# Kernel optimization log

Measured on AMD Instinct MI355X. Metric: run time of the kernel, lower is better.

## Reference

```python
import jax, jax.numpy as jnp
import numpy as np

N_NODES = 50000
N_EDGES = 800000
NFEATS = 256
HFEATS = 256
N_TARGET = 8
NEG_SLOPE = 0.2


def setup_inputs() -> dict:
    key = jax.random.key(0)
    ks = jax.random.split(key, 16)
    s = 1.0 / np.sqrt(HFEATS)
    inp = {
        'hv': jax.random.normal(ks[0], (N_NODES, NFEATS), dtype=jnp.float32),
        'src': jax.random.randint(ks[1], (N_EDGES,), 0, N_NODES, dtype=jnp.int32),
        'dst': jax.random.randint(ks[2], (N_EDGES,), 0, N_NODES, dtype=jnp.int32),
        'W_in': jax.random.normal(ks[3], (NFEATS, HFEATS), dtype=jnp.float32) * (1.0 / np.sqrt(NFEATS)),
        'b_in': jnp.zeros((HFEATS,), dtype=jnp.float32),
        'W_ro': jax.random.normal(ks[4], (3 * HFEATS, N_TARGET), dtype=jnp.float32) * (1.0 / np.sqrt(3 * HFEATS)),
        'b_ro': jnp.zeros((N_TARGET,), dtype=jnp.float32),
    }
    for i in range(1, 4):
        k = jax.random.split(ks[4 + i], 4)
        inp[f'fc{i}'] = jax.random.normal(k[0], (HFEATS, HFEATS), dtype=jnp.float32) * s
        inp[f'al{i}'] = jax.random.normal(k[1], (HFEATS,), dtype=jnp.float32) * s
        inp[f'ar{i}'] = jax.random.normal(k[2], (HFEATS,), dtype=jnp.float32) * s
        inp[f'bias{i}'] = jnp.zeros((HFEATS,), dtype=jnp.float32)
    return inp


def _gat(h, src, dst, fc, al, ar, bias):
    # DGL GATConv, 1 head: fc proj, additive attention, edge softmax over dst, sum agg.
    feat = h @ fc                                  # [N, H]
    el = feat @ al                                 # [N]
    er = feat @ ar                                 # [N]
    e = jax.nn.leaky_relu(el[src] + er[dst], NEG_SLOPE)   # [E]
    m = jax.ops.segment_max(e, dst, num_segments=N_NODES)
    ex = jnp.exp(e - m[dst])
    denom = jax.ops.segment_sum(ex, dst, num_segments=N_NODES)
    a = ex / denom[dst]                            # [E]
    out = jax.ops.segment_sum(feat[src] * a[:, None], dst, num_segments=N_NODES)
    return out + bias


def reference(hv, src, dst, W_in, b_in, W_ro, b_ro,
              fc1, al1, ar1, bias1, fc2, al2, ar2, bias2, fc3, al3, ar3, bias3):
    h0 = hv @ W_in + b_in
    h1 = _gat(jax.nn.relu(h0), src, dst, fc1, al1, ar1, bias1)
    h2 = _gat(jax.nn.relu(h1), src, dst, fc2, al2, ar2, bias2)
    h3 = _gat(jax.nn.relu(h2), src, dst, fc3, al3, ar3, bias3)
    out = jnp.concatenate([h1, h2, h3], axis=-1) @ W_ro + b_ro
    return jax.nn.sigmoid(out)
```

## Files before the change

kernel.cpp:

```cpp
#include <hip/hip_runtime.h>
#include <hip/hip_bf16.h>
#include <math.h>

#define NNODES 50000
#define NEDGES 800000
#define HF 256
#define NEG_SLOPE 0.2f
#define APAD 12288
#define CHUNK 3125
#define NBUCK 196
#define NG (NBUCK * 256)

typedef short bf16x8 __attribute__((ext_vector_type(8)));
typedef float f32x4 __attribute__((ext_vector_type(4)));
typedef float f32x2 __attribute__((ext_vector_type(2)));

__device__ __forceinline__ unsigned short f2bf(float f) {
  unsigned u = __float_as_uint(f);
  unsigned r = u + 0x7FFFu + ((u >> 16) & 1u);
  return (unsigned short)(r >> 16);
}
__device__ __forceinline__ float bf2f(unsigned short u) {
  return __uint_as_float((unsigned)u << 16);
}
__device__ __forceinline__ uint2 pack4(const float* v) {
  uint2 r;
  r.x = (unsigned)f2bf(v[0]) | ((unsigned)f2bf(v[1]) << 16);
  r.y = (unsigned)f2bf(v[2]) | ((unsigned)f2bf(v[3]) << 16);
  return r;
}
__device__ __forceinline__ uint4 pack8(const float* v) {
  uint4 r;
  r.x = (unsigned)f2bf(v[0]) | ((unsigned)f2bf(v[1]) << 16);
  r.y = (unsigned)f2bf(v[2]) | ((unsigned)f2bf(v[3]) << 16);
  r.z = (unsigned)f2bf(v[4]) | ((unsigned)f2bf(v[5]) << 16);
  r.w = (unsigned)f2bf(v[6]) | ((unsigned)f2bf(v[7]) << 16);
  return r;
}

__device__ __forceinline__ int permc(int p) {
  return (p & 192) | ((p & 3) << 4) | ((p & 63) >> 2);
}

#define GLOAD_LDS16(gsrc, ldst)                                                \
  __builtin_amdgcn_global_load_lds(                                           \
      (const __attribute__((address_space(1))) unsigned int*)(const void*)(gsrc), \
      (__attribute__((address_space(3))) unsigned int*)(void*)(ldst), 16, 0, 0)

__device__ __forceinline__ void slot_decode(int s, int& row, int& kb) {
  row = ((s >> 3) << 1) | (((s >> 2) & 1) ^ ((s >> 4) & 1));
  kb  = ((s & 1) ^ (row & 1)) | ((((s >> 1) & 1) ^ ((s >> 3) & 1)) << 1);
}

__global__ __launch_bounds__(256)
void conv_hv(const float* __restrict__ x, unsigned short* __restrict__ o) {
  size_t i = (size_t)(blockIdx.x * 256 + threadIdx.x) * 8;
  float4 a = *(const float4*)(x + i);
  float4 b = *(const float4*)(x + i + 4);
  float v[8] = {a.x, a.y, a.z, a.w, b.x, b.y, b.z, b.w};
  *(uint4*)(o + i) = pack8(v);
}

__global__ __launch_bounds__(256)
void conv_wt(const float* __restrict__ W0, const float* __restrict__ W1,
             const float* __restrict__ W2, const float* __restrict__ W3,
             unsigned short* __restrict__ WT) {
  int mat = blockIdx.y;
  const float* W = mat == 0 ? W0 : (mat == 1 ? W1 : (mat == 2 ? W2 : W3));
  int i = blockIdx.x * 256 + threadIdx.x;
  int n = i >> 8, p = i & 255;
  int k = (mat == 0) ? p : permc(p);
  WT[(size_t)mat * 65536 + i] = f2bf(W[(size_t)k * 256 + n]);
}

__global__ __launch_bounds__(256)
void conv_wro(const float* __restrict__ Wro, unsigned short* __restrict__ WroT) {
  int i = blockIdx.x * 256 + threadIdx.x;
  if (i >= 16 * 768) return;
  int n = i / 768, kk = i % 768;
  int part = kk >> 8, q = kk & 255;
  float v = (n < 8) ? Wro[(size_t)((part << 8) + permc(q)) * 8 + n] : 0.f;
  WroT[i] = f2bf(v);
}

template<bool BIAS_RELU, bool DOTS>
__global__ __launch_bounds__(256)
void gemm_bf16(const unsigned short* __restrict__ A, const unsigned short* __restrict__ WT,
               const float* __restrict__ bias,
               const float* __restrict__ al, const float* __restrict__ ar,
               void* __restrict__ Cv,
               float* __restrict__ el, float* __restrict__ er, int M) {
  __shared__ unsigned short As[2][64 * 32];
  __shared__ unsigned short Bs[2][256 * 32];
  __shared__ float sEl[64][4], sEr[64][4];
  const int t = threadIdx.x;
  const int lane = t & 63;
  const int w = t >> 6;
  const int wc = w * 64;
  const int brow = blockIdx.x * 64;

  f32x4 acc[4][4];
#pragma unroll
  for (int i = 0; i < 4; i++)
#pragma unroll
    for (int j = 0; j < 4; j++) acc[i][j] = (f32x4)(0.f);

  int rA, kA;
  slot_decode(w * 64 + lane, rA, kA);
  const unsigned short* aP = A + (size_t)(brow + rA) * 256 + kA * 8;
  const unsigned short* bP[4];
#pragma unroll
  for (int i = 0; i < 4; i++) {
    int rB, kB;
    slot_decode(w * 256 + i * 64 + lane, rB, kB);
    bP[i] = WT + (size_t)rB * 256 + kB * 8;
  }
  unsigned short* lA[2] = {&As[0][w * 512], &As[1][w * 512]};
  unsigned short* lB[2] = {&Bs[0][w * 2048], &Bs[1][w * 2048]};

#define STAGE(buf, kt)                                                         \
  do {                                                                         \
    GLOAD_LDS16(aP + (kt) * 32, lA[buf]);                                      \
    GLOAD_LDS16(bP[0] + (kt) * 32, lB[buf]);                                   \
    GLOAD_LDS16(bP[1] + (kt) * 32, lB[buf] + 512);                             \
    GLOAD_LDS16(bP[2] + (kt) * 32, lB[buf] + 1024);                            \
    GLOAD_LDS16(bP[3] + (kt) * 32, lB[buf] + 1536);                            \
  } while (0)

  const int fr = lane & 15, fq = lane >> 4;
  int ard[4], brd[4];
#pragma unroll
  for (int i = 0; i < 4; i++) {
    int rowA = i * 16 + fr;
    ard[i] = ((rowA * 64 + fq * 16) ^ ((rowA & 7) << 4));
    int rowB = wc + i * 16 + fr;
    brd[i] = ((rowB * 64 + fq * 16) ^ ((rowB & 7) << 4));
  }

  STAGE(0, 0);
  __syncthreads();
  int cur = 0;
#pragma unroll
  for (int kt = 0; kt < 8; kt++) {
    if (kt < 7) STAGE(cur ^ 1, kt + 1);
    bf16x8 af[4], bfr[4];
#pragma unroll
    for (int i = 0; i < 4; i++) {
      af[i]  = *(const bf16x8*)((const char*)As[cur] + ard[i]);
      bfr[i] = *(const bf16x8*)((const char*)Bs[cur] + brd[i]);
    }
#pragma unroll
    for (int i = 0; i < 4; i++)
#pragma unroll
      for (int j = 0; j < 4; j++)
        acc[i][j] = __builtin_amdgcn_mfma_f32_16x16x32_bf16(af[i], bfr[j], acc[i][j], 0, 0, 0);
    if (kt < 7) {
      __syncthreads();
      cur ^= 1;
    }
  }
#undef STAGE

#pragma unroll
  for (int i = 0; i < 4; i++) {
#pragma unroll
    for (int r = 0; r < 4; r++) {
      int row = brow + i * 16 + fq * 4 + r;
      if (row < M) {
        float v[4];
#pragma unroll
        for (int j = 0; j < 4; j++) {
          float x = acc[i][j][r];
          if (BIAS_RELU) x = fmaxf(x + bias[wc + j * 16 + fr], 0.f);
          v[j] = x;
        }
        if constexpr (DOTS) {
          int pk = __builtin_amdgcn_cvt_pk_fp8_f32(v[0], v[1], 0, false);
          pk = __builtin_amdgcn_cvt_pk_fp8_f32(v[2], v[3], pk, true);
          *(unsigned*)((unsigned char*)Cv + (size_t)row * 256 + wc + fr * 4) = (unsigned)pk;
        } else {
          *(uint2*)((unsigned short*)Cv + (size_t)row * 256 + wc + fr * 4) = pack4(v);
        }
      }
    }
  }

  if constexpr (DOTS) {
    float alv[4], arv[4];
#pragma unroll
    for (int j = 0; j < 4; j++) {
      int colj = wc + j * 16 + fr;
      alv[j] = al[colj];
      arv[j] = ar[colj];
    }
    float pel[16], per_[16];
#pragma unroll
    for (int i = 0; i < 4; i++)
#pragma unroll
      for (int r = 0; r < 4; r++) {
        float se = 0.f, sr = 0.f;
#pragma unroll
        for (int j = 0; j < 4; j++) {
          se = fmaf(acc[i][j][r], alv[j], se);
          sr = fmaf(acc[i][j][r], arv[j], sr);
        }
        pel[i * 4 + r] = se;
        per_[i * 4 + r] = sr;
      }
#pragma unroll
    for (int off = 1; off < 16; off <<= 1)
#pragma unroll
      for (int k = 0; k < 16; k++) {
        pel[k] += __shfl_xor(pel[k], off);
        per_[k] += __shfl_xor(per_[k], off);
      }
    if (fr == 0) {
#pragma unroll
      for (int i = 0; i < 4; i++)
#pragma unroll
        for (int r = 0; r < 4; r++) {
          int rl = i * 16 + fq * 4 + r;
          sEl[rl][w] = pel[i * 4 + r];
          sEr[rl][w] = per_[i * 4 + r];
        }
    }
    __syncthreads();
    if (t < 64) {
      int row = brow + t;
      if (row < M) {
        el[row] = sEl[t][0] + sEl[t][1] + sEl[t][2] + sEl[t][3];
        er[row] = sEr[t][0] + sEr[t][1] + sEr[t][2] + sEr[t][3];
      }
    }
  }
}

__global__ __launch_bounds__(256)
void hist_coarse(const int* __restrict__ dst, int* __restrict__ gh) {
  __shared__ int lh[NBUCK];
  const int t = threadIdx.x, blk = blockIdx.x;
  if (t < NBUCK) lh[t] = 0;
  __syncthreads();
  const int base = blk * CHUNK;
  for (int i = t; i < CHUNK; i += 256)
    atomicAdd(&lh[dst[base + i] >> 8], 1);
  __syncthreads();
  if (t < NBUCK) gh[t * 256 + blk] = lh[t];
}

__global__ __launch_bounds__(256)
void bsum2(const int* __restrict__ g, int* __restrict__ bsum) {
  __shared__ int sm[256];
  int t = threadIdx.x;
  sm[t] = g[blockIdx.x * 256 + t];
  __syncthreads();
  for (int off = 128; off; off >>= 1) {
    if (t < off) sm[t] += sm[t + off];
    __syncthreads();
  }
  if (t == 0) bsum[blockIdx.x] = sm[0];
}

__global__ __launch_bounds__(256)
void sscan2(const int* __restrict__ bsum, int* __restrict__ boff) {
  __shared__ int sm[256];
  int t = threadIdx.x;
  sm[t] = (t < NBUCK) ? bsum[t] : 0;
  __syncthreads();
  for (int o = 1; o < 256; o <<= 1) {
    int v = (t >= o) ? sm[t - o] : 0;
    __syncthreads();
    sm[t] += v;
    __syncthreads();
  }
  if (t < NBUCK) boff[t] = (t == 0) ? 0 : sm[t - 1];
}

__global__ __launch_bounds__(256)
void abase2(const int* __restrict__ g, const int* __restrict__ boff,
            int* __restrict__ abase) {
  __shared__ int sm[256];
  int t = threadIdx.x;
  int i = blockIdx.x * 256 + t;
  int v = g[i];
  sm[t] = v;
  __syncthreads();
  for (int o = 1; o < 256; o <<= 1) {
    int x = (t >= o) ? sm[t - o] : 0;
    __syncthreads();
    sm[t] += x;
    __syncthreads();
  }
  abase[i] = boff[blockIdx.x] + sm[t] - v;
}

__global__ __launch_bounds__(256)
void scatter_coarse(const int* __restrict__ src, const int* __restrict__ dst,
                    const int* __restrict__ abase, uint2* __restrict__ ebuf) {
  __shared__ int off[NBUCK];
  const int t = threadIdx.x, blk = blockIdx.x;
  if (t < NBUCK) off[t] = abase[t * 256 + blk];
  __syncthreads();
  const int base = blk * CHUNK;
  for (int i = t; i < CHUNK; i += 256) {
    int e = base + i;
    int d = dst[e], s = src[e];
    int p = atomicAdd(&off[d >> 8], 1);
    ebuf[p] = make_uint2((unsigned)s, (unsigned)d);
  }
}

__global__ __launch_bounds__(256)
void fine_sort(const uint2* __restrict__ ebuf, const int* __restrict__ abase,
               int* __restrict__ rowptr, int* __restrict__ col) {
  __shared__ int hist[256], pre[256], off[256];
  const int t = threadIdx.x, b = blockIdx.x;
  const int bstart = abase[b * 256];
  const int bend = (b < NBUCK - 1) ? abase[(b + 1) * 256] : NEDGES;
  hist[t] = 0;
  __syncthreads();
  for (int e = bstart + t; e < bend; e += 256)
    atomicAdd(&hist[ebuf[e].y & 255], 1);
  __syncthreads();
  pre[t] = hist[t];
  __syncthreads();
  for (int o = 1; o < 256; o <<= 1) {
    int v = (t >= o) ? pre[t - o] : 0;
    __syncthreads();
    pre[t] += v;
    __syncthreads();
  }
  const int excl = bstart + pre[t] - hist[t];
  const int node = b * 256 + t;
  if (node < NNODES) rowptr[node] = excl;
  if (node == NNODES - 1) rowptr[NNODES] = NEDGES;
  off[t] = excl;
  __syncthreads();
  for (int e = bstart + t; e < bend; e += 256) {
    uint2 ed = ebuf[e];
    int p = atomicAdd(&off[ed.y & 255], 1);
    col[p] = (int)ed.x;
  }
}

template<bool WRITE_RELU>
__global__ __launch_bounds__(256)
void gat_csr(const int* __restrict__ rowptr, const int* __restrict__ col,
             const float* __restrict__ el, const float* __restrict__ er,
             const unsigned char* __restrict__ feat8, const float* __restrict__ bias,
             unsigned short* __restrict__ h, unsigned short* __restrict__ hrelu) {
  int d = blockIdx.x * 4 + (threadIdx.x >> 6);
  int lane = threadIdx.x & 63;
  if (d >= NNODES) return;
  const int start = rowptr[d], end = rowptr[d + 1];
  float bv[4];
#pragma unroll
  for (int m = 0; m < 4; m++)
    bv[m] = bias[((lane >> 4) << 6) | (m << 4) | (lane & 15)];
  const size_t obase = (size_t)d * HF + lane * 4;
  if (start == end) {
    *(uint2*)(h + obase) = pack4(bv);
    if (WRITE_RELU) {
      float rv[4] = {fmaxf(bv[0], 0.f), fmaxf(bv[1], 0.f), fmaxf(bv[2], 0.f), fmaxf(bv[3], 0.f)};
      *(uint2*)(hrelu + obase) = pack4(rv);
    }
    return;
  }
  const float erd = er[d];

  float sm = 0.f;
  f32x2 acl = (f32x2)(0.f), ach = (f32x2)(0.f);

  for (int c0 = start; c0 < end; c0 += 64) {
    int j = c0 + lane;
    float ex = 0.f;
    int s = 0;
    if (j < end) {
      s = col[j];
      float x = el[s] + erd;
      x = x > 0.f ? x : NEG_SLOPE * x;
      ex = __expf(x);
    }
    sm += ex;
    int n = min(64, end - c0);
    for (int q = 0; q < n; q += 8) {
      int su[8];
      float eu[8];
#pragma unroll
      for (int u = 0; u < 8; u++) {
        su[u] = __builtin_amdgcn_readlane(s, q + u);
        eu[u] = __uint_as_float(
            (unsigned)__builtin_amdgcn_readlane((int)__float_as_uint(ex), q + u));
      }
      unsigned fv[8];
#pragma unroll
      for (int u = 0; u < 8; u++)
        fv[u] = *(const unsigned*)(feat8 + (size_t)su[u] * 256 + lane * 4);
#pragma unroll
      for (int u = 0; u < 8; u++) {
        f32x2 lo = __builtin_amdgcn_cvt_pk_f32_fp8((int)fv[u], false);
        f32x2 hi = __builtin_amdgcn_cvt_pk_f32_fp8((int)fv[u], true);
        f32x2 ev = {eu[u], eu[u]};
        acl = lo * ev + acl;
        ach = hi * ev + ach;
      }
    }
  }
#pragma unroll
  for (int off = 32; off; off >>= 1) sm += __shfl_xor(sm, off);

  const float rcp = 1.f / sm;
  float ov[4];
  ov[0] = fmaf(acl.x, rcp, bv[0]);
  ov[1] = fmaf(acl.y, rcp, bv[1]);
  ov[2] = fmaf(ach.x, rcp, bv[2]);
  ov[3] = fmaf(ach.y, rcp, bv[3]);
  *(uint2*)(h + obase) = pack4(ov);
  if (WRITE_RELU) {
    float rv[4] = {fmaxf(ov[0], 0.f), fmaxf(ov[1], 0.f), fmaxf(ov[2], 0.f), fmaxf(ov[3], 0.f)};
    *(uint2*)(hrelu + obase) = pack4(rv);
  }
}

__global__ __launch_bounds__(256)
void readout(const unsigned short* __restrict__ h1, const unsigned short* __restrict__ h2,
             const unsigned short* __restrict__ h3, const unsigned short* __restrict__ WroT,
             const float* __restrict__ bro, float* __restrict__ out) {
  const int t = threadIdx.x;
  const int lane = t & 63;
  const int w = t >> 6;
  const int fr = lane & 15, fq = lane >> 4;
  const int r0 = blockIdx.x * 64 + w * 16;
  if (r0 >= NNODES) return;
  const unsigned short* hs[3] = {h1, h2, h3};

  f32x4 acc = (f32x4)(0.f);
  const int koff = fq * 8;
#pragma unroll
  for (int part = 0; part < 3; ++part) {
    const unsigned short* hp = hs[part] + (size_t)(r0 + fr) * HF + koff;
    const unsigned short* wp = WroT + fr * 768 + part * 256 + koff;
#pragma unroll
    for (int kb = 0; kb < 8; ++kb) {
      bf16x8 af = *(const bf16x8*)(hp + kb * 32);
      bf16x8 bf = *(const bf16x8*)(wp + kb * 32);
      acc = __builtin_amdgcn_mfma_f32_16x16x32_bf16(af, bf, acc, 0, 0, 0);
    }
  }
  if (fr < 8) {
    const float b = bro[fr];
#pragma unroll
    for (int r = 0; r < 4; ++r) {
      int row = r0 + fq * 4 + r;
      float v = acc[r] + b;
      out[(size_t)row * 8 + fr] = 1.f / (1.f + expf(-v));
    }
  }
}

extern "C" void kernel_launch(void* const* d_in, const int* in_sizes, int n_in,
                              void* d_out, int out_size, void* d_ws, size_t ws_size,
                              hipStream_t stream) {
  const float* hv   = (const float*)d_in[0];
  const int*   src  = (const int*)d_in[1];
  const int*   dst  = (const int*)d_in[2];
  const float* W_in = (const float*)d_in[3];
  const float* b_in = (const float*)d_in[4];
  const float* W_ro = (const float*)d_in[5];
  const float* b_ro = (const float*)d_in[6];
  const float* fc[3]   = {(const float*)d_in[7],  (const float*)d_in[11], (const float*)d_in[15]};
  const float* al[3]   = {(const float*)d_in[8],  (const float*)d_in[12], (const float*)d_in[16]};
  const float* ar[3]   = {(const float*)d_in[9],  (const float*)d_in[13], (const float*)d_in[17]};
  const float* bias[3] = {(const float*)d_in[10], (const float*)d_in[14], (const float*)d_in[18]};
  float* out = (float*)d_out;

  const size_t NH = (size_t)NNODES * HF;
  unsigned short* h1    = (unsigned short*)d_ws;
  unsigned short* h2    = h1 + NH;
  unsigned short* h3    = h2 + NH;
  unsigned char*  feat8 = (unsigned char*)(h3 + NH);
  unsigned short* hrelu = (unsigned short*)(feat8 + NH);
  unsigned short* hvbf  = hrelu + NH + APAD;
  float* el   = (float*)(hvbf + NH + APAD);
  float* er   = el + NNODES;
  int* rowptr = (int*)(er + NNODES);
  int* gh     = rowptr + NNODES + 1;
  int* abase  = gh + NG;
  int* bsum   = abase + NG;
  int* boff   = bsum + 256;
  int* col    = boff + 256;
  uint2* ebuf = (uint2*)(col + NEDGES);
  unsigned short* WT = (unsigned short*)(ebuf + NEDGES);
  unsigned short* WroT = WT + 4 * 65536;

  const int gemm_grid = (NNODES + 63) / 64;
  const int gat_grid = (NNODES + 3) / 4;
  const int ro_grid = (NNODES + 63) / 64;

  conv_hv<<<(int)(NH / 2048), 256, 0, stream>>>(hv, hvbf);
  conv_wt<<<dim3(256, 4), 256, 0, stream>>>(W_in, fc[0], fc[1], fc[2], WT);
  conv_wro<<<48, 256, 0, stream>>>(W_ro, WroT);

  hist_coarse<<<256, 256, 0, stream>>>(dst, gh);
  bsum2<<<NBUCK, 256, 0, stream>>>(gh, bsum);
  sscan2<<<1, 256, 0, stream>>>(bsum, boff);
  abase2<<<NBUCK, 256, 0, stream>>>(gh, boff, abase);
  scatter_coarse<<<256, 256, 0, stream>>>(src, dst, abase, ebuf);
  fine_sort<<<NBUCK, 256, 0, stream>>>(ebuf, abase, rowptr, col);

  gemm_bf16<true, false><<<gemm_grid, 256, 0, stream>>>(
      hvbf, WT, b_in, nullptr, nullptr, hrelu, nullptr, nullptr, NNODES);

  unsigned short* houts[3] = {h1, h2, h3};
  for (int l = 0; l < 3; ++l) {
    unsigned short* hl = houts[l];
    gemm_bf16<false, true><<<gemm_grid, 256, 0, stream>>>(
        hrelu, WT + (size_t)(l + 1) * 65536, nullptr, al[l], ar[l], feat8, el, er, NNODES);
    if (l < 2)
      gat_csr<true><<<gat_grid, 256, 0, stream>>>(rowptr, col, el, er, feat8, bias[l], hl, hrelu);
    else
      gat_csr<false><<<gat_grid, 256, 0, stream>>>(rowptr, col, el, er, feat8, bias[l], hl, hrelu);
  }

  readout<<<ro_grid, 256, 0, stream>>>(h1, h2, h3, WroT, b_ro, out);
}
```

Baseline: 279.6 us.

## Replace LDS-staged GEMM with direct global-to-register MFMA loads per wave

The bf16 GEMM no longer stages A and W tiles through double-buffered LDS via global_load_lds. Each wave now computes 32 rows by all 256 columns, loading A fragments and the transposed weights straight from global memory into registers, with the weights expected to be served from cache. The el/er dot products are now reduced per wave with shuffles alone, removing the shared-memory cross-wave reduction and its barrier. In exchange each wave holds 32 accumulator vectors, raising register pressure (launch bounds set to 2 blocks), and the weights are re-read from global/L2 by every wave instead of being shared through LDS.

Result: slower. 334.7 us (+19.7%).

```diff
diff --git a/kernel.cpp b/kernel.cpp
--- a/kernel.cpp
+++ b/kernel.cpp
@@ -6,7 +6,6 @@
 #define NEDGES 800000
 #define HF 256
 #define NEG_SLOPE 0.2f
-#define APAD 12288
 #define CHUNK 3125
 #define NBUCK 196
 #define NG (NBUCK * 256)
@@ -40,16 +39,6 @@
 
 __device__ __forceinline__ int permc(int p) {
   return (p & 192) | ((p & 3) << 4) | ((p & 63) >> 2);
-}
-
-#define GLOAD_LDS16(gsrc, ldst)                                                \
-  __builtin_amdgcn_global_load_lds(                                           \
-      (const __attribute__((address_space(1))) unsigned int*)(const void*)(gsrc), \
-      (__attribute__((address_space(3))) unsigned int*)(void*)(ldst), 16, 0, 0)
-
-__device__ __forceinline__ void slot_decode(int s, int& row, int& kb) {
-  row = ((s >> 3) << 1) | (((s >> 2) & 1) ^ ((s >> 4) & 1));
-  kb  = ((s & 1) ^ (row & 1)) | ((((s >> 1) & 1) ^ ((s >> 3) & 1)) << 1);
 }
 
 __global__ __launch_bounds__(256)
@@ -84,152 +73,99 @@
 }
 
 template<bool BIAS_RELU, bool DOTS>
-__global__ __launch_bounds__(256)
+__global__ __launch_bounds__(256, 2)
 void gemm_bf16(const unsigned short* __restrict__ A, const unsigned short* __restrict__ WT,
                const float* __restrict__ bias,
                const float* __restrict__ al, const float* __restrict__ ar,
                void* __restrict__ Cv,
                float* __restrict__ el, float* __restrict__ er, int M) {
-  __shared__ unsigned short As[2][64 * 32];
-  __shared__ unsigned short Bs[2][256 * 32];
-  __shared__ float sEl[64][4], sEr[64][4];
   const int t = threadIdx.x;
   const int lane = t & 63;
   const int w = t >> 6;
-  const int wc = w * 64;
-  const int brow = blockIdx.x * 64;
-
-  f32x4 acc[4][4];
-#pragma unroll
-  for (int i = 0; i < 4; i++)
-#pragma unroll
-    for (int j = 0; j < 4; j++) acc[i][j] = (f32x4)(0.f);
-
-  int rA, kA;
-  slot_decode(w * 64 + lane, rA, kA);
-  const unsigned short* aP = A + (size_t)(brow + rA) * 256 + kA * 8;
-  const unsigned short* bP[4];
-#pragma unroll
-  for (int i = 0; i < 4; i++) {
-    int rB, kB;
-    slot_decode(w * 256 + i * 64 + lane, rB, kB);
-    bP[i] = WT + (size_t)rB * 256 + kB * 8;
-  }
-  unsigned short* lA[2] = {&As[0][w * 512], &As[1][w * 512]};
-  unsigned short* lB[2] = {&Bs[0][w * 2048], &Bs[1][w * 2048]};
-
-#define STAGE(buf, kt)                                                         \
-  do {                                                                         \
-    GLOAD_LDS16(aP + (kt) * 32, lA[buf]);                                      \
-    GLOAD_LDS16(bP[0] + (kt) * 32, lB[buf]);                                   \
-    GLOAD_LDS16(bP[1] + (kt) * 32, lB[buf] + 512);                             \
-    GLOAD_LDS16(bP[2] + (kt) * 32, lB[buf] + 1024);                            \
-    GLOAD_LDS16(bP[3] + (kt) * 32, lB[buf] + 1536);                            \
-  } while (0)
-
   const int fr = lane & 15, fq = lane >> 4;
-  int ard[4], brd[4];
-#pragma unroll
-  for (int i = 0; i < 4; i++) {
-    int rowA = i * 16 + fr;
-    ard[i] = ((rowA * 64 + fq * 16) ^ ((rowA & 7) << 4));
-    int rowB = wc + i * 16 + fr;
-    brd[i] = ((rowB * 64 + fq * 16) ^ ((rowB & 7) << 4));
-  }
-
-  STAGE(0, 0);
-  __syncthreads();
-  int cur = 0;
-#pragma unroll
-  for (int kt = 0; kt < 8; kt++) {
-    if (kt < 7) STAGE(cur ^ 1, kt + 1);
-    bf16x8 af[4], bfr[4];
-#pragma unroll
-    for (int i = 0; i < 4; i++) {
-      af[i]  = *(const bf16x8*)((const char*)As[cur] + ard[i]);
-      bfr[i] = *(const bf16x8*)((const char*)Bs[cur] + brd[i]);
-    }
-#pragma unroll
-    for (int i = 0; i < 4; i++)
-#pragma unroll
-      for (int j = 0; j < 4; j++)
-        acc[i][j] = __builtin_amdgcn_mfma_f32_16x16x32_bf16(af[i], bfr[j], acc[i][j], 0, 0, 0);
-    if (kt < 7) {
-      __syncthreads();
-      cur ^= 1;
-    }
-  }
-#undef STAGE
-
-#pragma unroll
-  for (int i = 0; i < 4; i++) {
+  const int r0 = blockIdx.x * 128 + w * 32;
+
+  const unsigned short* aP[2];
+#pragma unroll
+  for (int g = 0; g < 2; g++) {
+    int row = r0 + g * 16 + fr;
+    if (row >= M) row = M - 1;
+    aP[g] = A + (size_t)row * 256 + fq * 8;
+  }
+  const unsigned short* bP = WT + (size_t)fr * 256 + fq * 8;
+
+  f32x4 acc[2][16];
+#pragma unroll
+  for (int g = 0; g < 2; g++)
+#pragma unroll
+    for (int j = 0; j < 16; j++) acc[g][j] = (f32x4)(0.f);
+
+#pragma unroll 2
+  for (int step = 0; step < 8; step++) {
+    bf16x8 a0 = *(const bf16x8*)(aP[0] + step * 32);
+    bf16x8 a1 = *(const bf16x8*)(aP[1] + step * 32);
+#pragma unroll
+    for (int j = 0; j < 16; j++) {
+      bf16x8 bf = *(const bf16x8*)(bP + (size_t)j * 4096 + step * 32);
+      acc[0][j] = __builtin_amdgcn_mfma_f32_16x16x32_bf16(a0, bf, acc[0][j], 0, 0, 0);
+      acc[1][j] = __builtin_amdgcn_mfma_f32_16x16x32_bf16(a1, bf, acc[1][j], 0, 0, 0);
+    }
+  }
+
+#pragma unroll
+  for (int g = 0; g < 2; g++) {
 #pragma unroll
     for (int r = 0; r < 4; r++) {
-      int row = brow + i * 16 + fq * 4 + r;
+      int row = r0 + g * 16 + fq * 4 + r;
       if (row < M) {
-        float v[4];
-#pragma unroll
-        for (int j = 0; j < 4; j++) {
-          float x = acc[i][j][r];
-          if (BIAS_RELU) x = fmaxf(x + bias[wc + j * 16 + fr], 0.f);
-          v[j] = x;
-        }
-        if constexpr (DOTS) {
-          int pk = __builtin_amdgcn_cvt_pk_fp8_f32(v[0], v[1], 0, false);
-          pk = __builtin_amdgcn_cvt_pk_fp8_f32(v[2], v[3], pk, true);
-          *(unsigned*)((unsigned char*)Cv + (size_t)row * 256 + wc + fr * 4) = (unsigned)pk;
-        } else {
-          *(uint2*)((unsigned short*)Cv + (size_t)row * 256 + wc + fr * 4) = pack4(v);
+#pragma unroll
+        for (int w64 = 0; w64 < 4; w64++) {
+          float v[4];
+#pragma unroll
+          for (int jj = 0; jj < 4; jj++) {
+            float x = acc[g][w64 * 4 + jj][r];
+            if (BIAS_RELU) x = fmaxf(x + bias[(w64 * 4 + jj) * 16 + fr], 0.f);
+            v[jj] = x;
+          }
+          if constexpr (DOTS) {
+            int pk = __builtin_amdgcn_cvt_pk_fp8_f32(v[0], v[1], 0, false);
+            pk = __builtin_amdgcn_cvt_pk_fp8_f32(v[2], v[3], pk, true);
+            *(unsigned*)((unsigned char*)Cv + (size_t)row * 256 + w64 * 64 + fr * 4) = (unsigned)pk;
+          } else {
+            *(uint2*)((unsigned short*)Cv + (size_t)row * 256 + w64 * 64 + fr * 4) = pack4(v);
+          }
         }
       }
     }
   }
 
   if constexpr (DOTS) {
-    float alv[4], arv[4];
-#pragma unroll
-    for (int j = 0; j < 4; j++) {
-      int colj = wc + j * 16 + fr;
-      alv[j] = al[colj];
-      arv[j] = ar[colj];
-    }
-    float pel[16], per_[16];
-#pragma unroll
-    for (int i = 0; i < 4; i++)
+    float alv[16], arv[16];
+#pragma unroll
+    for (int j = 0; j < 16; j++) {
+      alv[j] = al[j * 16 + fr];
+      arv[j] = ar[j * 16 + fr];
+    }
+#pragma unroll
+    for (int g = 0; g < 2; g++) {
 #pragma unroll
       for (int r = 0; r < 4; r++) {
         float se = 0.f, sr = 0.f;
 #pragma unroll
-        for (int j = 0; j < 4; j++) {
-          se = fmaf(acc[i][j][r], alv[j], se);
-          sr = fmaf(acc[i][j][r], arv[j], sr);
+        for (int j = 0; j < 16; j++) {
+          se = fmaf(acc[g][j][r], alv[j], se);
+          sr = fmaf(acc[g][j][r], arv[j], sr);
         }
-        pel[i * 4 + r] = se;
-        per_[i * 4 + r] = sr;
-      }
-#pragma unroll
-    for (int off = 1; off < 16; off <<= 1)
-#pragma unroll
-      for (int k = 0; k < 16; k++) {
-        pel[k] += __shfl_xor(pel[k], off);
-        per_[k] += __shfl_xor(per_[k], off);
-      }
-    if (fr == 0) {
-#pragma unroll
-      for (int i = 0; i < 4; i++)
-#pragma unroll
-        for (int r = 0; r < 4; r++) {
-          int rl = i * 16 + fq * 4 + r;
-          sEl[rl][w] = pel[i * 4 + r];
-          sEr[rl][w] = per_[i * 4 + r];
+#pragma unroll
+        for (int off = 1; off < 16; off <<= 1) {
+          se += __shfl_xor(se, off);
+          sr += __shfl_xor(sr, off);
         }
-    }
-    __syncthreads();
-    if (t < 64) {
-      int row = brow + t;
-      if (row < M) {
-        el[row] = sEl[t][0] + sEl[t][1] + sEl[t][2] + sEl[t][3];
-        er[row] = sEr[t][0] + sEr[t][1] + sEr[t][2] + sEr[t][3];
+        int row = r0 + g * 16 + fq * 4 + r;
+        if (fr == 0 && row < M) {
+          el[row] = se;
+          er[row] = sr;
+        }
       }
     }
   }
@@ -480,8 +416,8 @@
   unsigned short* h3    = h2 + NH;
   unsigned char*  feat8 = (unsigned char*)(h3 + NH);
   unsigned short* hrelu = (unsigned short*)(feat8 + NH);
-  unsigned short* hvbf  = hrelu + NH + APAD;
-  float* el   = (float*)(hvbf + NH + APAD);
+  unsigned short* hvbf  = hrelu + NH;
+  float* el   = (float*)(hvbf + NH);
   float* er   = el + NNODES;
   int* rowptr = (int*)(er + NNODES);
   int* gh     = rowptr + NNODES + 1;
@@ -493,7 +429,7 @@
   unsigned short* WT = (unsigned short*)(ebuf + NEDGES);
   unsigned short* WroT = WT + 4 * 65536;
 
-  const int gemm_grid = (NNODES + 63) / 64;
+  const int gemm_grid = (NNODES + 127) / 128;
   const int gat_grid = (NNODES + 3) / 4;
   const int ro_grid = (NNODES + 63) / 64;
 
```

## Hold full weight matrix in LDS and read A fragments directly from global

Applied to the files above, without the earlier changes.

The GEMM kernel now loads the whole 256x256 bf16 weight matrix into LDS once per block (128 KB, swizzled) and uses 512-thread blocks covering 128 rows. A fragments are read straight from global memory into registers instead of being staged through double-buffered LDS. This drops the per-k-step barriers and A staging, and the APAD padding is removed by clamping out-of-range rows. In exchange occupancy falls to one block per CU and the A reads are uncoalesced global loads with no prefetch overlap.

New measurement: 294.9 us. 1.05x slower.

```diff
diff --git a/kernel.cpp b/kernel.cpp
--- a/kernel.cpp
+++ b/kernel.cpp
@@ -6,7 +6,6 @@
 #define NEDGES 800000
 #define HF 256
 #define NEG_SLOPE 0.2f
-#define APAD 12288
 #define CHUNK 3125
 #define NBUCK 196
 #define NG (NBUCK * 256)
@@ -46,11 +45,6 @@
   __builtin_amdgcn_global_load_lds(                                           \
       (const __attribute__((address_space(1))) unsigned int*)(const void*)(gsrc), \
       (__attribute__((address_space(3))) unsigned int*)(void*)(ldst), 16, 0, 0)
-
-__device__ __forceinline__ void slot_decode(int s, int& row, int& kb) {
-  row = ((s >> 3) << 1) | (((s >> 2) & 1) ^ ((s >> 4) & 1));
-  kb  = ((s & 1) ^ (row & 1)) | ((((s >> 1) & 1) ^ ((s >> 3) & 1)) << 1);
-}
 
 __global__ __launch_bounds__(256)
 void conv_hv(const float* __restrict__ x, unsigned short* __restrict__ o) {
@@ -84,20 +78,43 @@
 }
 
 template<bool BIAS_RELU, bool DOTS>
-__global__ __launch_bounds__(256)
+__global__ __launch_bounds__(512, 1)
 void gemm_bf16(const unsigned short* __restrict__ A, const unsigned short* __restrict__ WT,
                const float* __restrict__ bias,
                const float* __restrict__ al, const float* __restrict__ ar,
                void* __restrict__ Cv,
                float* __restrict__ el, float* __restrict__ er, int M) {
-  __shared__ unsigned short As[2][64 * 32];
-  __shared__ unsigned short Bs[2][256 * 32];
-  __shared__ float sEl[64][4], sEr[64][4];
+  __shared__ unsigned short Bs[256 * 256];
+  __shared__ float sEl[128][4], sEr[128][4];
   const int t = threadIdx.x;
   const int lane = t & 63;
   const int w = t >> 6;
-  const int wc = w * 64;
-  const int brow = blockIdx.x * 64;
+  const int band = w >> 2;
+  const int quad = w & 3;
+  const int fr = lane & 15, fq = lane >> 4;
+  const int brow = blockIdx.x * 128;
+
+  for (int i = 0; i < 16; i++) {
+    int s0 = (i * 8 + w) * 64;
+    int s = s0 + lane;
+    int g = (s & ~31) | ((s & 31) ^ ((s >> 5) & 7));
+    GLOAD_LDS16(WT + (size_t)g * 8, Bs + (size_t)s0 * 8);
+  }
+
+  const unsigned short* aP[4];
+#pragma unroll
+  for (int i = 0; i < 4; i++) {
+    int row = brow + band * 64 + i * 16 + fr;
+    if (row >= M) row = M - 1;
+    aP[i] = A + (size_t)row * 256 + fq * 8;
+  }
+  int blin[4], bxor[4];
+#pragma unroll
+  for (int j = 0; j < 4; j++) {
+    int n = quad * 64 + j * 16 + fr;
+    blin[j] = n * 512 + fq * 16;
+    bxor[j] = (n & 7) << 4;
+  }
 
   f32x4 acc[4][4];
 #pragma unroll
@@ -105,81 +122,42 @@
 #pragma unroll
     for (int j = 0; j < 4; j++) acc[i][j] = (f32x4)(0.f);
 
-  int rA, kA;
-  slot_decode(w * 64 + lane, rA, kA);
-  const unsigned short* aP = A + (size_t)(brow + rA) * 256 + kA * 8;
-  const unsigned short* bP[4];
-#pragma unroll
-  for (int i = 0; i < 4; i++) {
-    int rB, kB;
-    slot_decode(w * 256 + i * 64 + lane, rB, kB);
-    bP[i] = WT + (size_t)rB * 256 + kB * 8;
-  }
-  unsigned short* lA[2] = {&As[0][w * 512], &As[1][w * 512]};
-  unsigned short* lB[2] = {&Bs[0][w * 2048], &Bs[1][w * 2048]};
-
-#define STAGE(buf, kt)                                                         \
-  do {                                                                         \
-    GLOAD_LDS16(aP + (kt) * 32, lA[buf]);                                      \
-    GLOAD_LDS16(bP[0] + (kt) * 32, lB[buf]);                                   \
-    GLOAD_LDS16(bP[1] + (kt) * 32, lB[buf] + 512);                             \
-    GLOAD_LDS16(bP[2] + (kt) * 32, lB[buf] + 1024);                            \
-    GLOAD_LDS16(bP[3] + (kt) * 32, lB[buf] + 1536);                            \
-  } while (0)
-
-  const int fr = lane & 15, fq = lane >> 4;
-  int ard[4], brd[4];
-#pragma unroll
-  for (int i = 0; i < 4; i++) {
-    int rowA = i * 16 + fr;
-    ard[i] = ((rowA * 64 + fq * 16) ^ ((rowA & 7) << 4));
-    int rowB = wc + i * 16 + fr;
-    brd[i] = ((rowB * 64 + fq * 16) ^ ((rowB & 7) << 4));
-  }
-
-  STAGE(0, 0);
-  __syncthreads();
-  int cur = 0;
-#pragma unroll
-  for (int kt = 0; kt < 8; kt++) {
-    if (kt < 7) STAGE(cur ^ 1, kt + 1);
+  __syncthreads();
+
+#pragma unroll
+  for (int step = 0; step < 8; step++) {
     bf16x8 af[4], bfr[4];
 #pragma unroll
-    for (int i = 0; i < 4; i++) {
-      af[i]  = *(const bf16x8*)((const char*)As[cur] + ard[i]);
-      bfr[i] = *(const bf16x8*)((const char*)Bs[cur] + brd[i]);
-    }
+    for (int i = 0; i < 4; i++) af[i] = *(const bf16x8*)(aP[i] + step * 32);
+#pragma unroll
+    for (int j = 0; j < 4; j++)
+      bfr[j] = *(const bf16x8*)((const char*)Bs + ((blin[j] | (step << 6)) ^ bxor[j]));
 #pragma unroll
     for (int i = 0; i < 4; i++)
 #pragma unroll
       for (int j = 0; j < 4; j++)
         acc[i][j] = __builtin_amdgcn_mfma_f32_16x16x32_bf16(af[i], bfr[j], acc[i][j], 0, 0, 0);
-    if (kt < 7) {
-      __syncthreads();
-      cur ^= 1;
-    }
-  }
-#undef STAGE
+  }
 
 #pragma unroll
   for (int i = 0; i < 4; i++) {
 #pragma unroll
     for (int r = 0; r < 4; r++) {
-      int row = brow + i * 16 + fq * 4 + r;
+      int row = brow + band * 64 + i * 16 + fq * 4 + r;
       if (row < M) {
         float v[4];
 #pragma unroll
         for (int j = 0; j < 4; j++) {
           float x = acc[i][j][r];
-          if (BIAS_RELU) x = fmaxf(x + bias[wc + j * 16 + fr], 0.f);
+          if (BIAS_RELU) x = fmaxf(x + bias[quad * 64 + j * 16 + fr], 0.f);
           v[j] = x;
         }
         if constexpr (DOTS) {
           int pk = __builtin_amdgcn_cvt_pk_fp8_f32(v[0], v[1], 0, false);
           pk = __builtin_amdgcn_cvt_pk_fp8_f32(v[2], v[3], pk, true);
-          *(unsigned*)((unsigned char*)Cv + (size_t)row * 256 + wc + fr * 4) = (unsigned)pk;
+          *(unsigned*)((unsigned char*)Cv + (size_t)row * 256 + quad * 64 + fr * 4) = (unsigned)pk;
         } else {
-          *(uint2*)((unsigned short*)Cv + (size_t)row * 256 + wc + fr * 4) = pack4(v);
+          *(uint2*)((unsigned short*)Cv + (size_t)row * 256 + quad * 64 + fr * 4) = pack4(v);
         }
       }
     }
@@ -189,9 +167,9 @@
     float alv[4], arv[4];
 #pragma unroll
     for (int j = 0; j < 4; j++) {
-      int colj = wc + j * 16 + fr;
-      alv[j] = al[colj];
-      arv[j] = ar[colj];
+      int c = quad * 64 + j * 16 + fr;
+      alv[j] = al[c];
+      arv[j] = ar[c];
     }
     float pel[16], per_[16];
 #pragma unroll
@@ -219,13 +197,13 @@
       for (int i = 0; i < 4; i++)
 #pragma unroll
         for (int r = 0; r < 4; r++) {
-          int rl = i * 16 + fq * 4 + r;
-          sEl[rl][w] = pel[i * 4 + r];
-          sEr[rl][w] = per_[i * 4 + r];
+          int rl = band * 64 + i * 16 + fq * 4 + r;
+          sEl[rl][quad] = pel[i * 4 + r];
+          sEr[rl][quad] = per_[i * 4 + r];
         }
     }
     __syncthreads();
-    if (t < 64) {
+    if (t < 128) {
       int row = brow + t;
       if (row < M) {
         el[row] = sEl[t][0] + sEl[t][1] + sEl[t][2] + sEl[t][3];
@@ -480,8 +458,8 @@
   unsigned short* h3    = h2 + NH;
   unsigned char*  feat8 = (unsigned char*)(h3 + NH);
   unsigned short* hrelu = (unsigned short*)(feat8 + NH);
-  unsigned short* hvbf  = hrelu + NH + APAD;
-  float* el   = (float*)(hvbf + NH + APAD);
+  unsigned short* hvbf  = hrelu + NH;
+  float* el   = (float*)(hvbf + NH);
   float* er   = el + NNODES;
   int* rowptr = (int*)(er + NNODES);
   int* gh     = rowptr + NNODES + 1;
@@ -493,7 +471,7 @@
   unsigned short* WT = (unsigned short*)(ebuf + NEDGES);
   unsigned short* WroT = WT + 4 * 65536;
 
-  const int gemm_grid = (NNODES + 63) / 64;
+  const int gemm_grid = (NNODES + 127) / 128;
   const int gat_grid = (NNODES + 3) / 4;
   const int ro_grid = (NNODES + 63) / 64;
 
@@ -508,13 +486,13 @@
   scatter_coarse<<<256, 256, 0, stream>>>(src, dst, abase, ebuf);
   fine_sort<<<NBUCK, 256, 0, stream>>>(ebuf, abase, rowptr, col);
 
-  gemm_bf16<true, false><<<gemm_grid, 256, 0, stream>>>(
+  gemm_bf16<true, false><<<gemm_grid, 512, 0, stream>>>(
       hvbf, WT, b_in, nullptr, nullptr, hrelu, nullptr, nullptr, NNODES);
 
   unsigned short* houts[3] = {h1, h2, h3};
   for (int l = 0; l < 3; ++l) {
     unsigned short* hl = houts[l];
-    gemm_bf16<false, true><<<gemm_grid, 256, 0, stream>>>(
+    gemm_bf16<false, true><<<gemm_grid, 512, 0, stream>>>(
         hrelu, WT + (size_t)(l + 1) * 65536, nullptr, al[l], ar[l], feat8, el, er, NNODES);
     if (l < 2)
       gat_csr<true><<<gat_grid, 256, 0, stream>>>(rowptr, col, el, er, feat8, bias[l], hl, hrelu);
```
